# Optimization experiments

Measured on AMD Instinct MI355X. Metric: run time of the kernel, lower is better.

The kernel has to match this reference:

```python
import jax, jax.numpy as jnp
import numpy as np
import math

B, N, E = 32, 512, 8192          # graphs, nodes/graph, edges/graph
IN_DIM, D, H, HD, L, C = 64, 128, 4, 32, 3, 10
HID = 2 * D                      # _FeatureMLP hidden = max(d, 2*d)


def _ln(x, g, b, eps=1e-5):
    mu = x.mean(-1, keepdims=True)
    var = ((x - mu) ** 2).mean(-1, keepdims=True)
    return (x - mu) / jnp.sqrt(var + eps) * g + b


def _gelu(x):
    return jax.nn.gelu(x, approximate=False)  # torch nn.GELU default (erf)


def setup_inputs() -> dict:
    key = jax.random.key(0)
    ks = iter(jax.random.split(key, 48))
    def w(*shape):
        return jax.random.normal(next(ks), shape, jnp.float32) * 0.02
    z = lambda *s: jnp.zeros(s, jnp.float32)
    o = lambda *s: jnp.ones(s, jnp.float32)
    return {
        'x': jax.random.normal(next(ks), (B * N, IN_DIM), jnp.float32),
        'src': jax.random.randint(next(ks), (B, E), 0, N),
        'dst': jax.random.randint(next(ks), (B, E), 0, N),
        # node encoder: Linear -> LN -> GELU -> Linear -> LN
        'enc_w1': w(IN_DIM, HID), 'enc_b1': z(HID), 'enc_g1': o(HID), 'enc_bn1': z(HID),
        'enc_w2': w(HID, D), 'enc_b2': z(D), 'enc_g2': o(D), 'enc_bn2': z(D),
        # per-layer edge-message MLP (stacked over L)
        'msg_w1': w(L, 2 * D, D), 'msg_b1': z(L, D),
        'msg_w2': w(L, D, D), 'msg_b2': z(L, D),
        'msg_g': o(L, D), 'msg_bb': z(L, D),
        # per-layer attention
        'qw': w(L, D, H * HD), 'qb': z(L, H * HD),
        'kw': w(L, D, H * HD), 'kb': z(L, H * HD),
        'vw': w(L, D, H * HD), 'vb': z(L, H * HD),
        'ow': w(L, H * HD, D), 'ob': z(L, D),
        'attn_g': o(L, D), 'attn_b': z(L, D),
        # graph head: Linear(4d,2d) -> GELU -> LN -> Linear(2d,C)
        'gh_w1': w(4 * D, 2 * D), 'gh_b1': z(2 * D),
        'gh_g': o(2 * D), 'gh_bn': z(2 * D),
        'gh_w2': w(2 * D, C), 'gh_b2': z(C),
    }


def reference(x, src, dst, enc_w1, enc_b1, enc_g1, enc_bn1, enc_w2, enc_b2, enc_g2, enc_bn2,
              msg_w1, msg_b1, msg_w2, msg_b2, msg_g, msg_bb,
              qw, qb, kw, kb, vw, vb, ow, ob, attn_g, attn_b,
              gh_w1, gh_b1, gh_g, gh_bn, gh_w2, gh_b2):
    # node encoder
    t = _ln(x @ enc_w1 + enc_b1, enc_g1, enc_bn1)
    h = _ln(_gelu(t) @ enc_w2 + enc_b2, enc_g2, enc_bn2)
    h = h.reshape(B, N, D)
    seg = jax.vmap(lambda m, d: jax.ops.segment_sum(m, d, num_segments=N))
    for l in range(L):
        # edge message block: gather src/dst, MLP, scatter-add to dst
        hs = jnp.take_along_axis(h, src[..., None], axis=1)   # [B,E,D]
        hd = jnp.take_along_axis(h, dst[..., None], axis=1)   # [B,E,D]
        m = _gelu(jnp.concatenate([hs, hd], -1) @ msg_w1[l] + msg_b1[l]) @ msg_w2[l] + msg_b2[l]
        h = _ln(h + seg(m, dst), msg_g[l], msg_bb[l])
        # masked attention block (dense per-graph attention)
        q = (h @ qw[l] + qb[l]).reshape(B, N, H, HD)
        k = (h @ kw[l] + kb[l]).reshape(B, N, H, HD)
        v = (h @ vw[l] + vb[l]).reshape(B, N, H, HD)
        scores = jnp.einsum('bnhd,bmhd->bhnm', q, k) / math.sqrt(HD)
        attn = jax.nn.softmax(scores, axis=-1)
        o = jnp.einsum('bhnm,bmhd->bnhd', attn, v).reshape(B, N, H * HD)
        h = _ln(h + o @ ow[l] + ob[l], attn_g[l], attn_b[l])
    # graph pooling: mean | sum | max | std
    mean = h.mean(1)
    summ = h.sum(1)
    mx = h.max(1)
    std = jnp.sqrt(jax.nn.relu((h ** 2).mean(1) - mean ** 2) + 1e-6)
    pool = jnp.concatenate([mean, summ, mx, std], -1)         # [B,4D]
    g = _ln(_gelu(pool @ gh_w1 + gh_b1), gh_g, gh_bn)
    return g @ gh_w2 + gh_b2                                   # [B,C]
```

## Files before the change

### kernel.cpp

```cpp
#include <hip/hip_runtime.h>
#include <cmath>

#define B_   32
#define N_   512
#define E_   8192
#define BN_  16384
#define D_   128

typedef short bf16x8 __attribute__((ext_vector_type(8)));
typedef float f32x4  __attribute__((ext_vector_type(4)));

static __device__ __forceinline__ float bf2f(unsigned short u){
  union{unsigned int i; float f;} v; v.i = ((unsigned int)u)<<16; return v.f;
}
static __device__ __forceinline__ unsigned short f2bf(float f){
  union{unsigned int i; float f;} v; v.f=f;
  unsigned int x=v.i;
  return (unsigned short)((x + 0x7fffu + ((x>>16)&1u))>>16);
}
static __device__ __forceinline__ unsigned int pack2(float a, float b){
  return (unsigned int)f2bf(a) | ((unsigned int)f2bf(b)<<16);
}
static __device__ __forceinline__ float gelu_f(float x){
  float xs=x*0.70710678118654752f;
  float ax=fabsf(xs);
  float t=__builtin_amdgcn_rcpf(1.0f+0.3275911f*ax);
  float p=t*(0.254829592f+t*(-0.284496736f+t*(1.421413741f+t*(-1.453152027f+t*1.061405429f))));
  float er=1.0f - p*__expf(-ax*ax);
  er = (xs<0.f)? -er : er;
  return 0.5f*x*(1.0f+er);
}
static __device__ __forceinline__ float gelu_t(float x){
  float x2=x*x;
  float y=x*(-1.5957691216f + x2*(-0.0713548162f));
  float e=__expf(y);
  return x*__builtin_amdgcn_rcpf(1.0f+e);
}
static __device__ __forceinline__ float ldin(const void* p, size_t i, int isbf){
  return isbf ? bf2f(((const unsigned short*)p)[i]) : ((const float*)p)[i];
}

static __device__ __forceinline__ void block_sum2(float a, float b, float&A, float&Bv, float* red, int nw){
  int lane=threadIdx.x&63, w=threadIdx.x>>6;
  #pragma unroll
  for(int o=32;o>0;o>>=1){ a+=__shfl_down(a,o); b+=__shfl_down(b,o); }
  if(lane==0){ red[w]=a; red[8+w]=b; }
  __syncthreads();
  float sa=0.f, sb=0.f;
  for(int i=0;i<nw;i++){ sa+=red[i]; sb+=red[8+i]; }
  __syncthreads();
  A=sa; Bv=sb;
}

__global__ void sniff_kernel(const unsigned int* __restrict__ xw, int* __restrict__ flag){
  int t=threadIdx.x;
  int cnt=0;
  for(int i=0;i<32;i++){
    unsigned int w=xw[t+64*i];
    float v=bf2f((unsigned short)(w&0xffffu));
    float av=fabsf(v);
    if(v==0.0f || (av>=6e-5f && av<=8.0f)) cnt++;
  }
  #pragma unroll
  for(int o=32;o>0;o>>=1) cnt+=__shfl_down(cnt,o);
  if(t==0) *flag=(cnt>=1024)?1:0;
}

__global__ __launch_bounds__(256) void count_kernel(
  const int* __restrict__ dst, int* __restrict__ cnt)
{
  __shared__ int lc[512];
  int g=blockIdx.x, c=blockIdx.y, t=threadIdx.x;
  for(int i=t;i<512;i+=256) lc[i]=0;
  __syncthreads();
  for(int e=t;e<1024;e+=256) atomicAdd(&lc[dst[(size_t)g*E_+c*1024+e]],1);
  __syncthreads();
  for(int i=t;i<512;i+=256){ int v=lc[i]; if(v) atomicAdd(&cnt[g*512+i],v); }
}

__global__ __launch_bounds__(256) void scan_kernel(
  int* __restrict__ cnt, int* __restrict__ rowptr)
{
  __shared__ int sc[512];
  int g=blockIdx.x, t=threadIdx.x;
  for(int i=t;i<512;i+=256) sc[i]=cnt[g*512+i];
  __syncthreads();
  if(t==0){
    int acc=0;
    for(int i=0;i<512;i++){ int c=sc[i]; rowptr[g*513+i]=acc; cnt[g*512+i]=acc; acc+=c; }
    rowptr[g*513+512]=acc;
  }
}

__global__ __launch_bounds__(256) void scatter_kernel(
  const int* __restrict__ src, const int* __restrict__ dst,
  int* __restrict__ off, unsigned short* __restrict__ ss)
{
  int g=blockIdx.x, c=blockIdx.y, t=threadIdx.x;
  for(int e=t;e<1024;e+=256){
    size_t idx=(size_t)g*E_+c*1024+e;
    int d=dst[idx];
    int pos=atomicAdd(&off[g*512+d],1);
    ss[(size_t)g*E_+pos]=(unsigned short)src[idx];
  }
}

__global__ __launch_bounds__(256) void prep_kernel(
  const void* __restrict__ msg_w1, const void* __restrict__ msg_w2,
  const void* __restrict__ qw, const void* __restrict__ kw,
  const void* __restrict__ vw, const void* __restrict__ ow,
  const void* __restrict__ qb, const void* __restrict__ kb, const void* __restrict__ vb,
  const void* __restrict__ ob, const void* __restrict__ msg_b1, const void* __restrict__ msg_b2,
  const void* __restrict__ msg_g, const void* __restrict__ msg_bb,
  const void* __restrict__ attn_g, const void* __restrict__ attn_b,
  const void* __restrict__ enc_w1, const void* __restrict__ enc_w2,
  const void* __restrict__ enc_b1, const void* __restrict__ enc_g1, const void* __restrict__ enc_bn1,
  const void* __restrict__ enc_b2, const void* __restrict__ enc_g2, const void* __restrict__ enc_bn2,
  const void* __restrict__ gh_w1, const void* __restrict__ gh_w2,
  const void* __restrict__ gh_b1, const void* __restrict__ gh_g,
  const void* __restrict__ gh_bn, const void* __restrict__ gh_b2,
  unsigned short* __restrict__ w1t, unsigned short* __restrict__ w2k,
  unsigned short* __restrict__ qkvt, unsigned short* __restrict__ owt,
  unsigned short* __restrict__ w1te, unsigned short* __restrict__ w2te,
  unsigned short* __restrict__ ghw1t, unsigned short* __restrict__ ghw2t,
  unsigned short* __restrict__ cb, const int* __restrict__ flag)
{
  int isbf=*flag;
  int job=blockIdx.y;
  int i=blockIdx.x*256+threadIdx.x;
  if(job<3){
    if(i<32768){ int l=job; int k=i>>7, n=i&127; w1t[l*32768 + n*256 + k]=f2bf(ldin(msg_w1,(size_t)l*32768+i,isbf)); }
  } else if(job<6){
    int l=job-3; if(i<16384){ w2k[l*16384 + i]=f2bf(ldin(msg_w2,(size_t)l*16384+i,isbf)); }
  } else if(job<15){
    int r=job-6, l=r/3, which=r%3;
    if(i<16384){ int k=i>>7, n=i&127;
      const void* w=(which==0)?qw:((which==1)?kw:vw);
      qkvt[l*49152 + (which*128+n)*128 + k]=f2bf(ldin(w,(size_t)l*16384+i,isbf)); }
  } else if(job<18){
    int l=job-15; if(i<16384){ int k=i>>7, n=i&127; owt[l*16384 + n*128 + k]=f2bf(ldin(ow,(size_t)l*16384+i,isbf)); }
  } else if(job==18){
    if(i<3840){
      float v;
      if(i<1152){ int l=i/384, j=i%384, which=j>>7, jj=j&127;
        const void* bb=(which==0)?qb:((which==1)?kb:vb);
        v=ldin(bb,(size_t)l*128+jj,isbf);
      } else {
        int i2=i-1152; int r=i2/384; int rem=i2%384;
        const void* s = (r==0)?ob:((r==1)?msg_b1:((r==2)?msg_b2:((r==3)?msg_g:((r==4)?msg_bb:((r==5)?attn_g:attn_b)))));
        v=ldin(s,(size_t)rem,isbf);
      }
      cb[i]=f2bf(v);
    }
  } else if(job==19){
    if(i<1152){
      float v;
      if(i<256)       v=ldin(enc_b1,i,isbf);
      else if(i<512)  v=ldin(enc_g1,i-256,isbf);
      else if(i<768)  v=ldin(enc_bn1,i-512,isbf);
      else if(i<896)  v=ldin(enc_b2,i-768,isbf);
      else if(i<1024) v=ldin(enc_g2,i-896,isbf);
      else            v=ldin(enc_bn2,i-1024,isbf);
      cb[3840+i]=f2bf(v);
    }
  } else if(job==20){
    if(i<16384){ int k=i>>8, n=i&255; w1te[n*64+k]=f2bf(ldin(enc_w1,(size_t)i,isbf)); }
  } else if(job==21){
    if(i<32768){ int k=i>>7, n=i&127; w2te[n*256+k]=f2bf(ldin(enc_w2,(size_t)i,isbf)); }
  } else if(job<26){
    int p=job-22; int j=p*32768+i;
    if(i<32768){ int k=j>>8, n=j&255; ghw1t[n*512+k]=f2bf(ldin(gh_w1,(size_t)j,isbf)); }
  } else {
    if(i<2560){ int k=i/10, n=i%10; ghw2t[n*256+k]=f2bf(ldin(gh_w2,(size_t)i,isbf)); }
    else if(i<2560+778){
      int j=i-2560; float v;
      if(j<256)      v=ldin(gh_b1,j,isbf);
      else if(j<512) v=ldin(gh_g,j-256,isbf);
      else if(j<768) v=ldin(gh_bn,j-512,isbf);
      else           v=ldin(gh_b2,j-768,isbf);
      cb[4992+j]=f2bf(v);
    }
  }
}

__global__ __launch_bounds__(256) void enc_kernel(
  const void* __restrict__ x, const unsigned short* __restrict__ w1te,
  const unsigned short* __restrict__ w2te, const unsigned short* __restrict__ cb,
  unsigned short* __restrict__ h, const int* __restrict__ flag,
  const unsigned short* __restrict__ w1t0, unsigned short* __restrict__ UV)
{
  __shared__ __align__(16) unsigned short xs[64][72];
  __shared__ __align__(16) unsigned short t1[64][264];
  int isbf=*flag;
  int m0=blockIdx.x*64;
  int t=threadIdx.x, lane=t&63, w=t>>6, quad=lane>>4, ln=lane&15;
  for(int c2=t;c2<1024;c2+=256){
    int i=c2*4, row=i>>6, col=i&63;
    float v0,v1,v2,v3;
    if(isbf){
      const unsigned short* p=(const unsigned short*)x+(size_t)m0*64+i;
      v0=bf2f(p[0]); v1=bf2f(p[1]); v2=bf2f(p[2]); v3=bf2f(p[3]);
    } else {
      float4 f=*(const float4*)((const float*)x+(size_t)m0*64+i);
      v0=f.x; v1=f.y; v2=f.z; v3=f.w;
    }
    ushort4 o; o.x=f2bf(v0); o.y=f2bf(v1); o.z=f2bf(v2); o.w=f2bf(v3);
    *(ushort4*)&xs[row][col]=o;
  }
  __syncthreads();
  f32x4 a[4][4];
  #pragma unroll
  for(int nt=0;nt<4;nt++){ a[nt][0]={0,0,0,0}; a[nt][1]={0,0,0,0}; a[nt][2]={0,0,0,0}; a[nt][3]={0,0,0,0}; }
  #pragma unroll
  for(int k0i=0;k0i<2;k0i++){
    bf16x8 af[4];
    #pragma unroll
    for(int f=0;f<4;f++) af[f]=*(const bf16x8*)(&xs[f*16+ln][k0i*32+quad*8]);
    #pragma unroll
    for(int nt=0;nt<4;nt++){
      int n=w*64+nt*16+ln;
      bf16x8 bfr=*(const bf16x8*)(w1te+(size_t)n*64+k0i*32+quad*8);
      #pragma unroll
      for(int f=0;f<4;f++) a[nt][f]=__builtin_amdgcn_mfma_f32_16x16x32_bf16(af[f],bfr,a[nt][f],0,0,0);
    }
  }
  #pragma unroll
  for(int nt=0;nt<4;nt++){
    int n=w*64+nt*16+ln;
    float bv=bf2f(cb[3840+n]);
    #pragma unroll
    for(int f=0;f<4;f++)
      #pragma unroll
      for(int r=0;r<4;r++) t1[f*16+quad*4+r][n]=f2bf(a[nt][f][r]+bv);
  }
  __syncthreads();
  {
    int row=t>>2, qq=t&3;
    float s=0.f,s2=0.f;
    for(int c=qq*64;c<qq*64+64;c++){ float v=bf2f(t1[row][c]); s+=v; s2+=v*v; }
    s+=__shfl_xor(s,1); s+=__shfl_xor(s,2);
    s2+=__shfl_xor(s2,1); s2+=__shfl_xor(s2,2);
    float mu=s*(1.f/256.f), var=fmaxf(s2*(1.f/256.f)-mu*mu,0.f);
    float rr=rsqrtf(var+1e-5f);
    for(int c=qq*64;c<qq*64+64;c++){
      float v=bf2f(t1[row][c]);
      t1[row][c]=f2bf(gelu_f((v-mu)*rr*bf2f(cb[4096+c])+bf2f(cb[4352+c])));
    }
  }
  __syncthreads();
  f32x4 b2a[2][4];
  #pragma unroll
  for(int nt=0;nt<2;nt++){ b2a[nt][0]={0,0,0,0}; b2a[nt][1]={0,0,0,0}; b2a[nt][2]={0,0,0,0}; b2a[nt][3]={0,0,0,0}; }
  #pragma unroll
  for(int k0i=0;k0i<8;k0i++){
    bf16x8 af[4];
    #pragma unroll
    for(int f=0;f<4;f++) af[f]=*(const bf16x8*)(&t1[f*16+ln][k0i*32+quad*8]);
    #pragma unroll
    for(int nt=0;nt<2;nt++){
      int n=w*32+nt*16+ln;
      bf16x8 bfr=*(const bf16x8*)(w2te+(size_t)n*256+k0i*32+quad*8);
      #pragma unroll
      for(int f=0;f<4;f++) b2a[nt][f]=__builtin_amdgcn_mfma_f32_16x16x32_bf16(af[f],bfr,b2a[nt][f],0,0,0);
    }
  }
  __syncthreads();
  float* mf=(float*)&t1[0][0];
  #pragma unroll
  for(int nt=0;nt<2;nt++){
    int n=w*32+nt*16+ln;
    float bv=bf2f(cb[4608+n]);
    #pragma unroll
    for(int f=0;f<4;f++)
      #pragma unroll
      for(int r=0;r<4;r++) mf[(f*16+quad*4+r)*132+n]=b2a[nt][f][r]+bv;
  }
  __syncthreads();
  {
    int row=t>>2, qq=t&3;
    float vals[32];
    float s=0.f,s2=0.f;
    for(int j=0;j<32;j++){ float v=mf[row*132+qq*32+j]; vals[j]=v; s+=v; s2+=v*v; }
    s+=__shfl_xor(s,1); s+=__shfl_xor(s,2);
    s2+=__shfl_xor(s2,1); s2+=__shfl_xor(s2,2);
    float mu=s*(1.f/128.f), var=fmaxf(s2*(1.f/128.f)-mu*mu,0.f);
    float rr=rsqrtf(var+1e-5f);
    for(int j=0;j<32;j+=2){
      int c=qq*32+j;
      float v0=(vals[j]  -mu)*rr*bf2f(cb[4736+c  ])+bf2f(cb[4864+c  ]);
      float v1=(vals[j+1]-mu)*rr*bf2f(cb[4736+c+1])+bf2f(cb[4864+c+1]);
      *(unsigned int*)(h+(size_t)(m0+row)*128+c)=pack2(v0,v1);
      vals[j]=v0; vals[j+1]=v1;
    }
    __syncthreads();
    unsigned short* hb=&t1[0][0];
    for(int j=0;j<32;j++) hb[row*136+qq*32+j]=f2bf(vals[j]);
  }
  __syncthreads();
  {
    const unsigned short* hb=&t1[0][0];
    #pragma unroll
    for(int y=0;y<2;y++)
    #pragma unroll
    for(int nt=0;nt<2;nt++){
      int n=w*32+nt*16+ln;
      f32x4 a0={0,0,0,0},a1={0,0,0,0},a2={0,0,0,0},a3={0,0,0,0};
      const unsigned short* wp=w1t0+(size_t)n*256+y*128+quad*8;
      #pragma unroll
      for(int k0=0;k0<128;k0+=32){
        bf16x8 bfr=*(const bf16x8*)(wp+k0);
        bf16x8 f0=*(const bf16x8*)(hb+(size_t)(ln   )*136+k0+quad*8);
        bf16x8 f1=*(const bf16x8*)(hb+(size_t)(16+ln)*136+k0+quad*8);
        bf16x8 f2=*(const bf16x8*)(hb+(size_t)(32+ln)*136+k0+quad*8);
        bf16x8 f3=*(const bf16x8*)(hb+(size_t)(48+ln)*136+k0+quad*8);
        a0=__builtin_amdgcn_mfma_f32_16x16x32_bf16(f0,bfr,a0,0,0,0);
        a1=__builtin_amdgcn_mfma_f32_16x16x32_bf16(f1,bfr,a1,0,0,0);
        a2=__builtin_amdgcn_mfma_f32_16x16x32_bf16(f2,bfr,a2,0,0,0);
        a3=__builtin_amdgcn_mfma_f32_16x16x32_bf16(f3,bfr,a3,0,0,0);
      }
      float bv=y?0.f:bf2f(cb[1536+n]);
      #pragma unroll
      for(int r=0;r<4;r++){
        UV[(size_t)(m0   +quad*4+r)*256+y*128+n]=f2bf(a0[r]+bv);
        UV[(size_t)(m0+16+quad*4+r)*256+y*128+n]=f2bf(a1[r]+bv);
        UV[(size_t)(m0+32+quad*4+r)*256+y*128+n]=f2bf(a2[r]+bv);
        UV[(size_t)(m0+48+quad*4+r)*256+y*128+n]=f2bf(a3[r]+bv);
      }
    }
  }
}

__global__ __launch_bounds__(256) void qkvgen_kernel(
  const unsigned short* __restrict__ hrows, const unsigned short* __restrict__ wqkv,
  const unsigned short* __restrict__ bqkv,
  unsigned short* __restrict__ Qb, unsigned short* __restrict__ Kb,
  unsigned short* __restrict__ Vtb)
{
  __shared__ __align__(16) unsigned short a_t[64][136];
  int t=threadIdx.x;
  int m0=blockIdx.x*64;
  int y=blockIdx.y;
  for(int c=t;c<1024;c+=256){
    int m=c>>4, pp=c&15;
    *(uint4*)&a_t[m][pp*8]=*((const uint4*)(hrows+(size_t)(m0+m)*128)+pp);
  }
  __syncthreads();
  int lane=t&63, w=t>>6, quad=lane>>4, ln=lane&15;
  int gloc=m0>>9, r0=m0&511;
  #pragma unroll
  for(int nt=0;nt<2;nt++){
    int n=w*32+nt*16+ln;
    f32x4 a0={0,0,0,0},a1={0,0,0,0},a2={0,0,0,0},a3={0,0,0,0};
    const unsigned short* wp=wqkv+(size_t)(y*128+n)*128+quad*8;
    #pragma unroll
    for(int k0=0;k0<128;k0+=32){
      bf16x8 bfr=*(const bf16x8*)(wp+k0);
      bf16x8 f0=*(const bf16x8*)(&a_t[ln   ][k0+quad*8]);
      bf16x8 f1=*(const bf16x8*)(&a_t[16+ln][k0+quad*8]);
      bf16x8 f2=*(const bf16x8*)(&a_t[32+ln][k0+quad*8]);
      bf16x8 f3=*(const bf16x8*)(&a_t[48+ln][k0+quad*8]);
      a0=__builtin_amdgcn_mfma_f32_16x16x32_bf16(f0,bfr,a0,0,0,0);
      a1=__builtin_amdgcn_mfma_f32_16x16x32_bf16(f1,bfr,a1,0,0,0);
      a2=__builtin_amdgcn_mfma_f32_16x16x32_bf16(f2,bfr,a2,0,0,0);
      a3=__builtin_amdgcn_mfma_f32_16x16x32_bf16(f3,bfr,a3,0,0,0);
    }
    float bv=bf2f(bqkv[y*128+n]);
    if(y==0){
      const float sc=0.17677669529663689f;
      #pragma unroll
      for(int r=0;r<4;r++){
        Qb[(size_t)(m0   +quad*4+r)*128+n]=f2bf((a0[r]+bv)*sc);
        Qb[(size_t)(m0+16+quad*4+r)*128+n]=f2bf((a1[r]+bv)*sc);
        Qb[(size_t)(m0+32+quad*4+r)*128+n]=f2bf((a2[r]+bv)*sc);
        Qb[(size_t)(m0+48+quad*4+r)*128+n]=f2bf((a3[r]+bv)*sc);
      }
    } else if(y==1){
      #pragma unroll
      for(int r=0;r<4;r++){
        Kb[(size_t)(m0   +quad*4+r)*128+n]=f2bf(a0[r]+bv);
        Kb[(size_t)(m0+16+quad*4+r)*128+n]=f2bf(a1[r]+bv);
        Kb[(size_t)(m0+32+quad*4+r)*128+n]=f2bf(a2[r]+bv);
        Kb[(size_t)(m0+48+quad*4+r)*128+n]=f2bf(a3[r]+bv);
      }
    } else {
      unsigned short* vrow = Vtb + ((size_t)gloc*128+n)*512 + r0 + quad*4;
      ushort4 o;
      o.x=f2bf(a0[0]+bv); o.y=f2bf(a0[1]+bv); o.z=f2bf(a0[2]+bv); o.w=f2bf(a0[3]+bv);
      *(ushort4*)(vrow)=o;
      o.x=f2bf(a1[0]+bv); o.y=f2bf(a1[1]+bv); o.z=f2bf(a1[2]+bv); o.w=f2bf(a1[3]+bv);
      *(ushort4*)(vrow+16)=o;
      o.x=f2bf(a2[0]+bv); o.y=f2bf(a2[1]+bv); o.z=f2bf(a2[2]+bv); o.w=f2bf(a2[3]+bv);
      *(ushort4*)(vrow+32)=o;
      o.x=f2bf(a3[0]+bv); o.y=f2bf(a3[1]+bv); o.z=f2bf(a3[2]+bv); o.w=f2bf(a3[3]+bv);
      *(ushort4*)(vrow+48)=o;
    }
  }
}

__global__ __launch_bounds__(128) void edgef_kernel(
  unsigned short* __restrict__ h,
  const unsigned short* __restrict__ UV,
  const unsigned short* __restrict__ ss,
  const int* __restrict__ rowptr,
  const unsigned short* __restrict__ w2k,
  const unsigned short* __restrict__ b2,
  const unsigned short* __restrict__ gg, const unsigned short* __restrict__ bbp,
  int b0, int gEp)
{
  __shared__ __align__(16) float aggL[2][4][128];
  __shared__ __align__(16) float po[2][4][128];
  int t=threadIdx.x, lane=t&63, w=t>>6;
  int bid=blockIdx.x;
  int lg=bid%gEp, ch=bid/gEp;
  int g=b0+lg;
  const unsigned short* UVg = UV + (size_t)g*512*256;
  const unsigned short* ssg = ss + (size_t)g*E_;
  int dbase = ch*4;
  int bnd[5];
  #pragma unroll
  for(int i=0;i<5;i++) bnd[i]=rowptr[g*513+dbase+i];
  #pragma unroll 1
  for(int dd=0;dd<4;dd++){
    int e_lo=bnd[dd], e_hi0=bnd[dd+1];
    int half=(e_hi0-e_lo+1)>>1;
    int es = w ? (e_lo+half) : e_lo;
    int ee = w ? e_hi0       : (e_lo+half);
    unsigned int vdw=*(const unsigned int*)(UVg + (size_t)(dbase+dd)*256 + 128 + lane*2);
    float v0=bf2f((unsigned short)(vdw&0xffffu)), v1=bf2f((unsigned short)(vdw>>16));
    float a0=0.f, a1=0.f;
    int si3,si4,si5;
    unsigned int u0,u1,u2;
    {
      int s0=__builtin_amdgcn_readfirstlane((int)ssg[es  ])&511;
      int s1=__builtin_amdgcn_readfirstlane((int)ssg[es+1])&511;
      int s2=__builtin_amdgcn_readfirstlane((int)ssg[es+2])&511;
      si3=(int)ssg[es+3]; si4=(int)ssg[es+4]; si5=(int)ssg[es+5];
      u0=*(const unsigned int*)(UVg + (size_t)s0*256 + lane*2);
      u1=*(const unsigned int*)(UVg + (size_t)s1*256 + lane*2);
      u2=*(const unsigned int*)(UVg + (size_t)s2*256 + lane*2);
    }
    #pragma unroll 2
    for(int e=es;e<ee;e++){
      float z0=bf2f((unsigned short)(u0&0xffffu))+v0;
      float z1=bf2f((unsigned short)(u0>>16))+v1;
      u0=u1; u1=u2;
      int s3=__builtin_amdgcn_readfirstlane(si3)&511;
      u2=*(const unsigned int*)(UVg + (size_t)s3*256 + lane*2);
      si3=si4; si4=si5;
      si5=(int)ssg[e+6];
      a0+=gelu_t(z0); a1+=gelu_t(z1);
    }
    aggL[w][dd][lane*2  ]=a0;
    aggL[w][dd][lane*2+1]=a1;
  }
  __syncthreads();
  float o[4][2];
  #pragma unroll
  for(int dd=0;dd<4;dd++){ o[dd][0]=0.f; o[dd][1]=0.f; }
  #pragma unroll 4
  for(int kk=0;kk<64;kk++){
    int k=w*64+kk;
    unsigned int wdw=*(const unsigned int*)(w2k+(size_t)k*128+lane*2);
    float w0=bf2f((unsigned short)(wdw&0xffffu));
    float w1=bf2f((unsigned short)(wdw>>16));
    #pragma unroll
    for(int dd=0;dd<4;dd++){
      float av=aggL[0][dd][k]+aggL[1][dd][k];
      o[dd][0]+=av*w0; o[dd][1]+=av*w1;
    }
  }
  #pragma unroll
  for(int dd=0;dd<4;dd++){
    po[w][dd][lane*2  ]=o[dd][0];
    po[w][dd][lane*2+1]=o[dd][1];
  }
  __syncthreads();
  #pragma unroll 1
  for(int p=0;p<2;p++){
    int di=w*2+p;
    int d = dbase + di;
    float deg=(float)(bnd[di+1]-bnd[di]);
    float o0=bf2f(b2[lane*2  ])*deg + po[0][di][lane*2  ] + po[1][di][lane*2  ];
    float o1=bf2f(b2[lane*2+1])*deg + po[0][di][lane*2+1] + po[1][di][lane*2+1];
    size_t base=(size_t)(g*512+d)*128;
    unsigned int hdw=*(const unsigned int*)(h+base+lane*2);
    float x0=bf2f((unsigned short)(hdw&0xffffu))+o0;
    float x1=bf2f((unsigned short)(hdw>>16))+o1;
    float s1=x0+x1, s2=x0*x0+x1*x1;
    #pragma unroll
    for(int off=32;off>0;off>>=1){ s1+=__shfl_xor(s1,off); s2+=__shfl_xor(s2,off); }
    float mu=s1*(1.f/128.f), var=fmaxf(s2*(1.f/128.f)-mu*mu,0.f);
    float rr=rsqrtf(var+1e-5f);
    float y0=(x0-mu)*rr*bf2f(gg[lane*2  ])+bf2f(bbp[lane*2  ]);
    float y1=(x1-mu)*rr*bf2f(gg[lane*2+1])+bf2f(bbp[lane*2+1]);
    *(unsigned int*)(h+base+lane*2)=pack2(y0,y1);
  }
}

__global__ __launch_bounds__(256) void attn_fused_kernel(
  const unsigned short* __restrict__ Qb, const unsigned short* __restrict__ Kb,
  const unsigned short* __restrict__ Vtb,
  const unsigned short* __restrict__ wo, const unsigned short* __restrict__ bo,
  unsigned short* __restrict__ h,
  const unsigned short* __restrict__ gg, const unsigned short* __restrict__ bbp,
  const unsigned short* __restrict__ w1tn, const unsigned short* __restrict__ b1n,
  unsigned short* __restrict__ UV, int b0, int gA, int do_uv)
{
  __shared__ __align__(16) unsigned short hO[32][136];
  __shared__ __align__(16) unsigned short Psh[4][16][72];
  __shared__ __align__(16) float mf[32][132];
  int bx=blockIdx.x;
  int lg=bx%gA, ch=bx/gA;
  int r0=ch*32;
  int g=b0+lg;
  int t=threadIdx.x, lane=t&63, w=t>>6, quad=lane>>4, ln=lane&15;
  const unsigned short* Qg = Qb + (size_t)lg*65536;
  const unsigned short* Kg = Kb + (size_t)lg*65536 + w*32;
  const unsigned short* Vg = Vtb + ((size_t)lg*128 + w*32)*512;
  bf16x8 qf[2];
  #pragma unroll
  for(int qt=0;qt<2;qt++)
    qf[qt]=*(const bf16x8*)(Qg + (size_t)(r0+qt*16+ln)*128 + w*32 + quad*8);
  f32x4 O[2][2]; float Lp[2][4];
  #pragma unroll
  for(int qt=0;qt<2;qt++){ O[qt][0]={0,0,0,0}; O[qt][1]={0,0,0,0};
    #pragma unroll
    for(int r=0;r<4;r++) Lp[qt][r]=0.f; }
  for(int kc=0;kc<8;kc++){
    bf16x8 kf[4];
    #pragma unroll
    for(int f=0;f<4;f++) kf[f]=*(const bf16x8*)(Kg + (size_t)(kc*64+f*16+ln)*128 + quad*8);
    bf16x8 va[2], vb[2];
    #pragma unroll
    for(int s2=0;s2<2;s2++){
      va[s2]=*(const bf16x8*)(Vg + (size_t)ln*512      + kc*64 + s2*32 + quad*8);
      vb[s2]=*(const bf16x8*)(Vg + (size_t)(16+ln)*512 + kc*64 + s2*32 + quad*8);
    }
    #pragma unroll
    for(int qt=0;qt<2;qt++){
      f32x4 s[4];
      #pragma unroll
      for(int f=0;f<4;f++){
        f32x4 z={0,0,0,0};
        s[f]=__builtin_amdgcn_mfma_f32_16x16x32_bf16(qf[qt],kf[f],z,0,0,0);
      }
      #pragma unroll
      for(int f=0;f<4;f++)
        #pragma unroll
        for(int r=0;r<4;r++){
          float pe=__expf(fminf(s[f][r],30.0f));
          Psh[w][quad*4+r][f*16+ln]=f2bf(pe);
          Lp[qt][r]+=pe;
        }
      #pragma unroll
      for(int s2=0;s2<2;s2++){
        bf16x8 pf=*(const bf16x8*)(&Psh[w][ln][s2*32+quad*8]);
        O[qt][0]=__builtin_amdgcn_mfma_f32_16x16x32_bf16(pf,va[s2],O[qt][0],0,0,0);
        O[qt][1]=__builtin_amdgcn_mfma_f32_16x16x32_bf16(pf,vb[s2],O[qt][1],0,0,0);
      }
    }
  }
  #pragma unroll
  for(int qt=0;qt<2;qt++){
    #pragma unroll
    for(int o=1;o<16;o<<=1)
      #pragma unroll
      for(int r=0;r<4;r++) Lp[qt][r]+=__shfl_xor(Lp[qt][r],o);
    #pragma unroll
    for(int r=0;r<4;r++){
      float inv=1.0f/Lp[qt][r];
      int qr=qt*16+quad*4+r;
      hO[qr][w*32+ln   ]=f2bf(O[qt][0][r]*inv);
      hO[qr][w*32+16+ln]=f2bf(O[qt][1][r]*inv);
    }
  }
  __syncthreads();
  #pragma unroll
  for(int nt=0;nt<2;nt++){
    int n=w*32+nt*16+ln;
    f32x4 a0={0,0,0,0},a1={0,0,0,0};
    const unsigned short* wp=wo+(size_t)n*128+quad*8;
    #pragma unroll
    for(int k0=0;k0<128;k0+=32){
      bf16x8 bfr=*(const bf16x8*)(wp+k0);
      bf16x8 f0=*(const bf16x8*)(&hO[ln   ][k0+quad*8]);
      bf16x8 f1=*(const bf16x8*)(&hO[16+ln][k0+quad*8]);
      a0=__builtin_amdgcn_mfma_f32_16x16x32_bf16(f0,bfr,a0,0,0,0);
      a1=__builtin_amdgcn_mfma_f32_16x16x32_bf16(f1,bfr,a1,0,0,0);
    }
    float bv=bf2f(bo[n]);
    #pragma unroll
    for(int r=0;r<4;r++){
      mf[quad*4+r   ][n]=a0[r]+bv;
      mf[16+quad*4+r][n]=a1[r]+bv;
    }
  }
  __syncthreads();
  {
    int row=t>>3, oct=t&7;
    size_t base=((size_t)(g*512+r0+row))*128;
    float vals[16];
    float s=0.f,s2=0.f;
    for(int j=0;j<16;j++){
      int c=oct*16+j;
      float v=bf2f(h[base+c])+mf[row][c];
      vals[j]=v; s+=v; s2+=v*v;
    }
    s+=__shfl_xor(s,1); s+=__shfl_xor(s,2); s+=__shfl_xor(s,4);
    s2+=__shfl_xor(s2,1); s2+=__shfl_xor(s2,2); s2+=__shfl_xor(s2,4);
    float mu=s*(1.f/128.f), var=fmaxf(s2*(1.f/128.f)-mu*mu,0.f);
    float rr=rsqrtf(var+1e-5f);
    for(int j=0;j<16;j+=2){
      int c=oct*16+j;
      float y0=(vals[j]  -mu)*rr*bf2f(gg[c  ])+bf2f(bbp[c  ]);
      float y1=(vals[j+1]-mu)*rr*bf2f(gg[c+1])+bf2f(bbp[c+1]);
      *(unsigned int*)(h+base+c)=pack2(y0,y1);
      hO[row][c]=f2bf(y0); hO[row][c+1]=f2bf(y1);
    }
  }
  if(!do_uv) return;
  __syncthreads();
  #pragma unroll
  for(int y=0;y<2;y++)
  #pragma unroll
  for(int nt=0;nt<2;nt++){
    int n=w*32+nt*16+ln;
    f32x4 a0={0,0,0,0},a1={0,0,0,0};
    const unsigned short* wp=w1tn+(size_t)n*256+y*128+quad*8;
    #pragma unroll
    for(int k0=0;k0<128;k0+=32){
      bf16x8 bfr=*(const bf16x8*)(wp+k0);
      bf16x8 f0=*(const bf16x8*)(&hO[ln   ][k0+quad*8]);
      bf16x8 f1=*(const bf16x8*)(&hO[16+ln][k0+quad*8]);
      a0=__builtin_amdgcn_mfma_f32_16x16x32_bf16(f0,bfr,a0,0,0,0);
      a1=__builtin_amdgcn_mfma_f32_16x16x32_bf16(f1,bfr,a1,0,0,0);
    }
    float bv=y?0.f:bf2f(b1n[n]);
    size_t rb=(size_t)(g*512+r0);
    #pragma unroll
    for(int r=0;r<4;r++){
      UV[(rb   +quad*4+r)*256+y*128+n]=f2bf(a0[r]+bv);
      UV[(rb+16+quad*4+r)*256+y*128+n]=f2bf(a1[r]+bv);
    }
  }
}

__global__ __launch_bounds__(256) void poolp_kernel(
  const unsigned short* __restrict__ h, float* __restrict__ part)
{
  __shared__ float ps[256], ps2[256], pm[256];
  int b=blockIdx.x, c=blockIdx.y;
  int t=threadIdx.x, d=t&127, hf=t>>7;
  float s=0.f,s2=0.f,mx=-1e30f;
  for(int r=hf*32;r<hf*32+32;r++){
    float v=bf2f(h[((size_t)(b*512+c*64+r))*128+d]);
    s+=v; s2+=v*v; mx=fmaxf(mx,v);
  }
  ps[t]=s; ps2[t]=s2; pm[t]=mx;
  __syncthreads();
  if(t<128){
    s=ps[t]+ps[128+t]; s2=ps2[t]+ps2[128+t]; mx=fmaxf(pm[t],pm[128+t]);
    size_t base=((size_t)(b*8+c))*384;
    part[base+t]=s; part[base+128+t]=s2; part[base+256+t]=mx;
  }
}

__global__ __launch_bounds__(256) void head_kernel(
  const float* __restrict__ part, const unsigned short* __restrict__ ghw1t,
  const unsigned short* __restrict__ ghw2t, const unsigned short* __restrict__ cb,
  void* __restrict__ out, const int* __restrict__ flag)
{
  int isbf=*flag;
  int b=blockIdx.x, t=threadIdx.x;
  __shared__ float pl[512];
  __shared__ float gl[256];
  __shared__ float red[16];
  if(t<128){
    float s=0.f,s2=0.f,mx=-1e30f;
    for(int c=0;c<8;c++){
      size_t base=((size_t)(b*8+c))*384;
      s += part[base+t];
      s2+= part[base+128+t];
      mx = fmaxf(mx, part[base+256+t]);
    }
    float mean=s*(1.f/512.f);
    float var=fmaxf(s2*(1.f/512.f)-mean*mean,0.f);
    float sd=sqrtf(var+1e-6f);
    pl[t]=mean; pl[128+t]=s; pl[256+t]=mx; pl[384+t]=sd;
  }
  __syncthreads();
  float a=bf2f(cb[4992+t]);
  const unsigned short* wr=ghw1t+(size_t)t*512;
  for(int k0=0;k0<512;k0+=8){
    bf16x8 wv=*(const bf16x8*)(wr+k0);
    const unsigned short* wp=(const unsigned short*)&wv;
    #pragma unroll
    for(int j=0;j<8;j++) a+=pl[k0+j]*bf2f(wp[j]);
  }
  float u=gelu_f(a);
  float S,S2; block_sum2(u,u*u,S,S2,red,4);
  float mu=S*(1.f/256.f), var=fmaxf(S2*(1.f/256.f)-mu*mu,0.f);
  float r=rsqrtf(var+1e-5f);
  gl[t]=(u-mu)*r*bf2f(cb[5248+t])+bf2f(cb[5504+t]);
  __syncthreads();
  if(t<10){
    float o=bf2f(cb[5760+t]);
    const unsigned short* wr2=ghw2t+(size_t)t*256;
    for(int k0=0;k0<256;k0+=8){
      bf16x8 wv=*(const bf16x8*)(wr2+k0);
      const unsigned short* wp=(const unsigned short*)&wv;
      #pragma unroll
      for(int j=0;j<8;j++) o+=gl[k0+j]*bf2f(wp[j]);
    }
    if(isbf) ((unsigned short*)out)[b*10+t]=f2bf(o);
    else     ((float*)out)[b*10+t]=o;
  }
}

extern "C" void kernel_launch(void* const* d_in, const int* in_sizes, int n_in,
                              void* d_out, int out_size, void* d_ws, size_t ws_size,
                              hipStream_t stream)
{
  const void* x      =d_in[0];
  const int*  src    =(const int*)d_in[1];
  const int*  dstp   =(const int*)d_in[2];
  const void* enc_w1 =d_in[3];  const void* enc_b1 =d_in[4];
  const void* enc_g1 =d_in[5];  const void* enc_bn1=d_in[6];
  const void* enc_w2 =d_in[7];  const void* enc_b2 =d_in[8];
  const void* enc_g2 =d_in[9];  const void* enc_bn2=d_in[10];
  const void* msg_w1 =d_in[11]; const void* msg_b1 =d_in[12];
  const void* msg_w2 =d_in[13]; const void* msg_b2 =d_in[14];
  const void* msg_g  =d_in[15]; const void* msg_bb =d_in[16];
  const void* qw     =d_in[17]; const void* qb     =d_in[18];
  const void* kw     =d_in[19]; const void* kb     =d_in[20];
  const void* vw     =d_in[21]; const void* vb     =d_in[22];
  const void* ow     =d_in[23]; const void* ob     =d_in[24];
  const void* attn_g =d_in[25]; const void* attn_b =d_in[26];
  const void* gh_w1  =d_in[27]; const void* gh_b1  =d_in[28];
  const void* gh_g   =d_in[29]; const void* gh_bn  =d_in[30];
  const void* gh_w2  =d_in[31]; const void* gh_b2  =d_in[32];
  (void)in_sizes; (void)n_in; (void)out_size;

  char* base=(char*)d_ws;
  unsigned short* h    =(unsigned short*)(base);
  unsigned short* w1t  =(unsigned short*)(base + 4194304);
  unsigned short* w2k  =(unsigned short*)(base + 4390912);
  unsigned short* qkvt =(unsigned short*)(base + 4489216);
  unsigned short* owt  =(unsigned short*)(base + 4784128);
  unsigned short* w1te =(unsigned short*)(base + 4882432);
  unsigned short* w2te =(unsigned short*)(base + 4915200);
  unsigned short* ghw1t=(unsigned short*)(base + 4980736);
  unsigned short* ghw2t=(unsigned short*)(base + 5242880);
  unsigned short* cb   =(unsigned short*)(base + 5248000);
  int*   rowptr        =(int*)(base + 5325312);
  int*   flag          =(int*)(base + 5390976);
  int*   cnt           =(int*)(base + 5391360);
  unsigned short* ssrt =(unsigned short*)(base + 5505024);
  char* R              = base + 6029312;

  size_t Rcap = (ws_size > 6029312) ? (ws_size - 6029312) : 0;
  int gA = 32;
  while(gA > 4 && 8388608 + (size_t)gA*393216 > Rcap) gA >>= 1;
  int apass = 32/gA;
  unsigned short* UV  =(unsigned short*)R;
  unsigned short* Qb  =UV  + 4194304;
  unsigned short* Kb  =Qb  + (size_t)gA*65536;
  unsigned short* Vtb =Kb  + (size_t)gA*65536;
  float* part=(float*)R;

  sniff_kernel<<<1,64,0,stream>>>((const unsigned int*)x, flag);
  hipMemsetAsync(cnt,0,65536,stream);
  count_kernel<<<dim3(B_,8),256,0,stream>>>(dstp,cnt);
  scan_kernel<<<B_,256,0,stream>>>(cnt,rowptr);
  scatter_kernel<<<dim3(B_,8),256,0,stream>>>(src,dstp,cnt,ssrt);
  prep_kernel<<<dim3(128,27),256,0,stream>>>(msg_w1,msg_w2,qw,kw,vw,ow,qb,kb,vb,
      ob,msg_b1,msg_b2,msg_g,msg_bb,attn_g,attn_b,
      enc_w1,enc_w2,enc_b1,enc_g1,enc_bn1,enc_b2,enc_g2,enc_bn2,
      gh_w1,gh_w2,gh_b1,gh_g,gh_bn,gh_b2,
      w1t,w2k,qkvt,owt,w1te,w2te,ghw1t,ghw2t,cb,flag);

  enc_kernel<<<BN_/64,256,0,stream>>>(x,w1te,w2te,cb,h,flag,w1t,UV);

  for(int l=0;l<3;l++){
    edgef_kernel<<<32*128,128,0,stream>>>(h,UV,ssrt,rowptr,
        w2k+(size_t)l*16384, cb+1920+l*128, cb+2304+l*128, cb+2688+l*128, 0, 32);
    int ln=(l+1)%3;
    for(int ap=0;ap<apass;ap++){
      int b0=ap*gA;
      qkvgen_kernel<<<dim3(gA*8,3),256,0,stream>>>(h+(size_t)b0*512*128,
          qkvt+(size_t)l*49152, cb+l*384, Qb, Kb, Vtb);
      attn_fused_kernel<<<gA*16,256,0,stream>>>(Qb, Kb, Vtb,
          owt+(size_t)l*16384, cb+1152+l*128, h, cb+3072+l*128, cb+3456+l*128,
          w1t+(size_t)ln*32768, cb+1536+ln*128, UV, b0, gA, (l<2)?1:0);
    }
  }
  poolp_kernel<<<dim3(B_,8),256,0,stream>>>(h,part);
  head_kernel<<<B_,256,0,stream>>>(part,ghw1t,ghw2t,cb,d_out,flag);
}
```

Measured before the change: 387.9 us.

## Merge edge-sort preprocessing into one kernel and fuse pooling into final attention

Replaces the sniff, count, scan and scatter kernels and the memset with a single sort kernel. It uses one block per graph, shared-memory histograms and a wave-shuffle prefix scan instead of a serial scan; an extra block runs the dtype sniff. Graph pooling partials (sum, sum of squares, max) are now computed in the last-layer attention kernel from the freshly normalized rows, which removes the separate pool kernel and its re-read of h. This cuts launch count and memory traffic. In exchange, the sort phase runs on only 33 blocks, and the partials go into the UV workspace region.

```diff
diff --git a/kernel.cpp b/kernel.cpp
--- a/kernel.cpp
+++ b/kernel.cpp
@@ -52,56 +52,59 @@
   A=sa; Bv=sb;
 }
 
-__global__ void sniff_kernel(const unsigned int* __restrict__ xw, int* __restrict__ flag){
+__global__ __launch_bounds__(256) void sort_kernel(
+  const int* __restrict__ src, const int* __restrict__ dst,
+  int* __restrict__ rowptr, unsigned short* __restrict__ ss,
+  const unsigned int* __restrict__ xw, int* __restrict__ flag)
+{
   int t=threadIdx.x;
-  int cnt=0;
-  for(int i=0;i<32;i++){
-    unsigned int w=xw[t+64*i];
-    float v=bf2f((unsigned short)(w&0xffffu));
-    float av=fabsf(v);
-    if(v==0.0f || (av>=6e-5f && av<=8.0f)) cnt++;
-  }
-  #pragma unroll
-  for(int o=32;o>0;o>>=1) cnt+=__shfl_down(cnt,o);
-  if(t==0) *flag=(cnt>=1024)?1:0;
-}
-
-__global__ __launch_bounds__(256) void count_kernel(
-  const int* __restrict__ dst, int* __restrict__ cnt)
-{
-  __shared__ int lc[512];
-  int g=blockIdx.x, c=blockIdx.y, t=threadIdx.x;
-  for(int i=t;i<512;i+=256) lc[i]=0;
-  __syncthreads();
-  for(int e=t;e<1024;e+=256) atomicAdd(&lc[dst[(size_t)g*E_+c*1024+e]],1);
-  __syncthreads();
-  for(int i=t;i<512;i+=256){ int v=lc[i]; if(v) atomicAdd(&cnt[g*512+i],v); }
-}
-
-__global__ __launch_bounds__(256) void scan_kernel(
-  int* __restrict__ cnt, int* __restrict__ rowptr)
-{
-  __shared__ int sc[512];
-  int g=blockIdx.x, t=threadIdx.x;
-  for(int i=t;i<512;i+=256) sc[i]=cnt[g*512+i];
-  __syncthreads();
-  if(t==0){
-    int acc=0;
-    for(int i=0;i<512;i++){ int c=sc[i]; rowptr[g*513+i]=acc; cnt[g*512+i]=acc; acc+=c; }
-    rowptr[g*513+512]=acc;
-  }
-}
-
-__global__ __launch_bounds__(256) void scatter_kernel(
-  const int* __restrict__ src, const int* __restrict__ dst,
-  int* __restrict__ off, unsigned short* __restrict__ ss)
-{
-  int g=blockIdx.x, c=blockIdx.y, t=threadIdx.x;
-  for(int e=t;e<1024;e+=256){
-    size_t idx=(size_t)g*E_+c*1024+e;
-    int d=dst[idx];
-    int pos=atomicAdd(&off[g*512+d],1);
-    ss[(size_t)g*E_+pos]=(unsigned short)src[idx];
+  if(blockIdx.x==32){
+    if(t<64){
+      int cnt=0;
+      for(int i=0;i<32;i++){
+        unsigned int w=xw[t+64*i];
+        float v=bf2f((unsigned short)(w&0xffffu));
+        float av=fabsf(v);
+        if(v==0.0f || (av>=6e-5f && av<=8.0f)) cnt++;
+      }
+      #pragma unroll
+      for(int o=32;o>0;o>>=1) cnt+=__shfl_down(cnt,o);
+      if(t==0) *flag=(cnt>=1024)?1:0;
+    }
+    return;
+  }
+  __shared__ int cnts[512];
+  __shared__ int offs[512];
+  __shared__ int wred[8];
+  int g=blockIdx.x;
+  for(int i=t;i<512;i+=256) cnts[i]=0;
+  __syncthreads();
+  const int* dg=dst+(size_t)g*E_;
+  for(int e=t;e<E_;e+=256) atomicAdd(&cnts[dg[e]],1);
+  __syncthreads();
+  int lane=t&63, w=t>>6;
+  int c0=cnts[2*t], c1=cnts[2*t+1];
+  int mysum=c0+c1;
+  int sc=mysum;
+  #pragma unroll
+  for(int o=1;o<64;o<<=1){ int v=__shfl_up(sc,o); if(lane>=o) sc+=v; }
+  if(lane==63) wred[w]=sc;
+  __syncthreads();
+  int wbase=0;
+  for(int i=0;i<w;i++) wbase+=wred[i];
+  int excl=wbase+sc-mysum;
+  rowptr[g*513+2*t  ]=excl;
+  rowptr[g*513+2*t+1]=excl+c0;
+  offs[2*t  ]=excl;
+  offs[2*t+1]=excl+c0;
+  if(t==255) rowptr[g*513+512]=wbase+sc;
+  __syncthreads();
+  const int* sg=src+(size_t)g*E_;
+  unsigned short* ssg=ss+(size_t)g*E_;
+  for(int e=t;e<E_;e+=256){
+    int d=dg[e];
+    int pos=atomicAdd(&offs[d],1);
+    ssg[pos]=(unsigned short)sg[e];
   }
 }
 
@@ -504,7 +507,7 @@
   unsigned short* __restrict__ h,
   const unsigned short* __restrict__ gg, const unsigned short* __restrict__ bbp,
   const unsigned short* __restrict__ w1tn, const unsigned short* __restrict__ b1n,
-  unsigned short* __restrict__ UV, int b0, int gA, int do_uv)
+  unsigned short* __restrict__ UV, float* part, int b0, int gA, int do_uv)
 {
   __shared__ __align__(16) unsigned short hO[32][136];
   __shared__ __align__(16) unsigned short Psh[4][16][72];
@@ -616,10 +619,19 @@
       float y1=(vals[j+1]-mu)*rr*bf2f(gg[c+1])+bf2f(bbp[c+1]);
       *(unsigned int*)(h+base+c)=pack2(y0,y1);
       hO[row][c]=f2bf(y0); hO[row][c+1]=f2bf(y1);
-    }
-  }
-  if(!do_uv) return;
-  __syncthreads();
+      mf[row][c]=y0; mf[row][c+1]=y1;
+    }
+  }
+  __syncthreads();
+  if(!do_uv){
+    if(t<128){
+      float s=0.f,s2=0.f,mx=-1e30f;
+      for(int r=0;r<32;r++){ float v=mf[r][t]; s+=v; s2+=v*v; mx=fmaxf(mx,v); }
+      size_t pb=((size_t)(g*16+ch))*384;
+      part[pb+t]=s; part[pb+128+t]=s2; part[pb+256+t]=mx;
+    }
+    return;
+  }
   #pragma unroll
   for(int y=0;y<2;y++)
   #pragma unroll
@@ -642,26 +654,6 @@
       UV[(rb   +quad*4+r)*256+y*128+n]=f2bf(a0[r]+bv);
       UV[(rb+16+quad*4+r)*256+y*128+n]=f2bf(a1[r]+bv);
     }
-  }
-}
-
-__global__ __launch_bounds__(256) void poolp_kernel(
-  const unsigned short* __restrict__ h, float* __restrict__ part)
-{
-  __shared__ float ps[256], ps2[256], pm[256];
-  int b=blockIdx.x, c=blockIdx.y;
-  int t=threadIdx.x, d=t&127, hf=t>>7;
-  float s=0.f,s2=0.f,mx=-1e30f;
-  for(int r=hf*32;r<hf*32+32;r++){
-    float v=bf2f(h[((size_t)(b*512+c*64+r))*128+d]);
-    s+=v; s2+=v*v; mx=fmaxf(mx,v);
-  }
-  ps[t]=s; ps2[t]=s2; pm[t]=mx;
-  __syncthreads();
-  if(t<128){
-    s=ps[t]+ps[128+t]; s2=ps2[t]+ps2[128+t]; mx=fmaxf(pm[t],pm[128+t]);
-    size_t base=((size_t)(b*8+c))*384;
-    part[base+t]=s; part[base+128+t]=s2; part[base+256+t]=mx;
   }
 }
 
@@ -677,8 +669,8 @@
   __shared__ float red[16];
   if(t<128){
     float s=0.f,s2=0.f,mx=-1e30f;
-    for(int c=0;c<8;c++){
-      size_t base=((size_t)(b*8+c))*384;
+    for(int c=0;c<16;c++){
+      size_t base=((size_t)(b*16+c))*384;
       s += part[base+t];
       s2+= part[base+128+t];
       mx = fmaxf(mx, part[base+256+t]);
@@ -754,7 +746,6 @@
   unsigned short* cb   =(unsigned short*)(base + 5248000);
   int*   rowptr        =(int*)(base + 5325312);
   int*   flag          =(int*)(base + 5390976);
-  int*   cnt           =(int*)(base + 5391360);
   unsigned short* ssrt =(unsigned short*)(base + 5505024);
   char* R              = base + 6029312;
 
@@ -768,11 +759,7 @@
   unsigned short* Vtb =Kb  + (size_t)gA*65536;
   float* part=(float*)R;
 
-  sniff_kernel<<<1,64,0,stream>>>((const unsigned int*)x, flag);
-  hipMemsetAsync(cnt,0,65536,stream);
-  count_kernel<<<dim3(B_,8),256,0,stream>>>(dstp,cnt);
-  scan_kernel<<<B_,256,0,stream>>>(cnt,rowptr);
-  scatter_kernel<<<dim3(B_,8),256,0,stream>>>(src,dstp,cnt,ssrt);
+  sort_kernel<<<33,256,0,stream>>>(src,dstp,rowptr,ssrt,(const unsigned int*)x,flag);
   prep_kernel<<<dim3(128,27),256,0,stream>>>(msg_w1,msg_w2,qw,kw,vw,ow,qb,kb,vb,
       ob,msg_b1,msg_b2,msg_g,msg_bb,attn_g,attn_b,
       enc_w1,enc_w2,enc_b1,enc_g1,enc_bn1,enc_b2,enc_g2,enc_bn2,
@@ -791,9 +778,8 @@
           qkvt+(size_t)l*49152, cb+l*384, Qb, Kb, Vtb);
       attn_fused_kernel<<<gA*16,256,0,stream>>>(Qb, Kb, Vtb,
           owt+(size_t)l*16384, cb+1152+l*128, h, cb+3072+l*128, cb+3456+l*128,
-          w1t+(size_t)ln*32768, cb+1536+ln*128, UV, b0, gA, (l<2)?1:0);
-    }
-  }
-  poolp_kernel<<<dim3(B_,8),256,0,stream>>>(h,part);
+          w1t+(size_t)ln*32768, cb+1536+ln*128, UV, part, b0, gA, (l<2)?1:0);
+    }
+  }
   head_kernel<<<B_,256,0,stream>>>(part,ghw1t,ghw2t,cb,d_out,flag);
 }
```

After: 383.3 us. About the same (-1.2%).
